# Performance work log

Measured on AMD Instinct MI355X. Metric: run time of the kernel, lower is better.

Reference implementation:

```python
import jax, jax.numpy as jnp
import numpy as np

VOCAB, B, T, E, H, C = 50000, 1024, 120, 50, 300, 5
FORGET_BIAS = 1.0  # tf.nn.rnn_cell.LSTMCell default


def setup_inputs() -> dict:
    key = jax.random.key(0)
    ks = jax.random.split(key, 8)
    tokens = jax.random.randint(ks[0], (B, T, 1), 0, VOCAB, dtype=jnp.int32)
    labels = jax.random.randint(ks[1], (B, T), 0, C, dtype=jnp.int32)
    mask = jax.random.randint(ks[2], (B, T), 0, 2, dtype=jnp.int32).astype(bool)
    embeddings = jax.random.normal(ks[3], (VOCAB, E), dtype=jnp.float32) * 0.1
    Wx = jax.random.normal(ks[4], (E, 4 * H), dtype=jnp.float32) * (1.0 / np.sqrt(E))
    Wh = jax.random.normal(ks[5], (H, 4 * H), dtype=jnp.float32) * (1.0 / np.sqrt(H))
    b = jnp.zeros((4 * H,), dtype=jnp.float32)
    U = jax.random.normal(ks[6], (H, C), dtype=jnp.float32) * (1.0 / np.sqrt(H))
    b2 = jnp.zeros((C,), dtype=jnp.float32)
    return {"tokens": tokens, "labels": labels, "mask": mask,
            "embeddings": embeddings, "Wx": Wx, "Wh": Wh, "b": b, "U": U, "b2": b2}


def reference(tokens, labels, mask, embeddings, Wx, Wh, b, U, b2):
    # Embedding lookup: (B, T, n_features=1) -> (B, T, E)
    x = embeddings[tokens[..., 0]]

    def step(carry, xt):
        c, h = carry
        z = xt @ Wx + h @ Wh + b           # (B, 4H), gate order i, j, f, o
        i, j, f, o = jnp.split(z, 4, axis=-1)
        c_new = jax.nn.sigmoid(f + FORGET_BIAS) * c + jax.nn.sigmoid(i) * jnp.tanh(j)
        h_new = jax.nn.sigmoid(o) * jnp.tanh(c_new)
        return (c_new, h_new), h_new

    nb = x.shape[0]
    c0 = jnp.zeros((nb, H), dtype=x.dtype)
    h0 = jnp.zeros((nb, H), dtype=x.dtype)
    _, hs = jax.lax.scan(step, (c0, h0), jnp.swapaxes(x, 0, 1))  # (T, B, H)
    hs = jnp.swapaxes(hs, 0, 1)                                   # (B, T, H)

    logits = hs @ U + b2                                          # (B, T, C)
    logp = jax.nn.log_softmax(logits, axis=-1)
    ce = -jnp.take_along_axis(logp, labels[..., None].astype(jnp.int32), axis=-1)[..., 0]
    m = mask.astype(ce.dtype)
    loss = jnp.sum(ce * m) / jnp.sum(m)  # mean over unmasked tokens
    return loss
```

## Files before the change

kernel.cpp:

```cpp
#include <hip/hip_runtime.h>
#include <hip/hip_bf16.h>
#include <math.h>

#define NBATCH 1024
#define NT 120
#define NE 50
#define NH 300
#define NC 5
#define GH 1200
#define NKPAD 352
#define NSTRIP 15
#define HS 20
#define SCOL 80
#define NGRP 16
#define BB 64
#define ASTR 360
#define WSTR 360
#define ZSTR 84
#define HBSTR 304
#define HCH 76
#define NCHUNK 4800

typedef __attribute__((ext_vector_type(8))) short short8;
typedef __attribute__((ext_vector_type(4))) float f32x4;
typedef __attribute__((ext_vector_type(2))) unsigned short us2;

static __device__ __forceinline__ float bf2f(unsigned short u) {
    unsigned int x = ((unsigned int)u) << 16;
    return __builtin_bit_cast(float, x);
}
static __device__ __forceinline__ unsigned short f2bf(float f) {
    __hip_bfloat16 h = __float2bfloat16(f);
    return __builtin_bit_cast(unsigned short, h);
}

__global__ __launch_bounds__(256)
void wswz_kernel(const float* __restrict__ Wx, const float* __restrict__ Wh,
                 unsigned short* __restrict__ Wswz)
{
    int idx = blockIdx.x * 256 + threadIdx.x;
    if (idx >= NSTRIP * SCOL * NKPAD) return;
    int s = idx / (SCOL * NKPAD);
    int r = idx % (SCOL * NKPAD);
    int j = r / NKPAD, k = r % NKPAD;
    int col = (j & 3) * NH + s * HS + (j >> 2);
    float v = 0.f;
    if (k < NH)           v = Wh[k * GH + col];
    else if (k < NH + NE) v = Wx[(k - NH) * GH + col];
    Wswz[idx] = f2bf(v);
}

__device__ __forceinline__ void load_h(const unsigned short* __restrict__ hb,
                                       int b0, unsigned short* A_s, int tid)
{
    const unsigned long long* src =
        (const unsigned long long*)(hb + (size_t)b0 * HBSTR);
    unsigned long long v[19];
#pragma unroll
    for (int m = 0; m < 19; ++m) {
        const int idx = tid + 256 * m;
        if (idx < NCHUNK) {
            const int row = idx / 75, j = idx % 75;
            v[m] = __hip_atomic_load(src + (size_t)row * HCH + j,
                                     __ATOMIC_RELAXED, __HIP_MEMORY_SCOPE_AGENT);
        }
    }
#pragma unroll
    for (int m = 0; m < 19; ++m) {
        const int idx = tid + 256 * m;
        if (idx < NCHUNK) {
            const int row = idx / 75, j = idx % 75;
            *(unsigned long long*)(A_s + row * ASTR + j * 4) = v[m];
        }
    }
}

__device__ __forceinline__ void store_h(unsigned short* hb, int b0, int st,
                                        const unsigned short* h_stage, int tid)
{
#pragma unroll
    for (int m = 0; m < 2; ++m) {
        const int c = tid + m * 256;
        if (c < 320) {
            const int row = c / 5, j = c % 5;
            unsigned long long val =
                *(const unsigned long long*)(h_stage + row * HS + j * 4);
            unsigned long long* p = (unsigned long long*)
                (hb + (size_t)(b0 + row) * HBSTR + st * HS + j * 4);
            __hip_atomic_store(p, val, __ATOMIC_RELAXED,
                               __HIP_MEMORY_SCOPE_AGENT);
        }
    }
}

__device__ __forceinline__ void load_x(const int* __restrict__ tokens,
                                       const float* __restrict__ emb,
                                       int b0, int t, unsigned short* A_s, int tid)
{
    const int row = tid >> 2, q = tid & 3;
    const int tok = tokens[(b0 + row) * NT + t];
    const float* er = emb + (size_t)tok * NE;
    unsigned short* dst = A_s + row * ASTR + NH;
    for (int m = 0; m < 7; ++m) {
        int f = q + 4 * m;
        if (f < 25) {
            float2 v = *(const float2*)(er + f * 2);
            us2 o; o.x = f2bf(v.x); o.y = f2bf(v.y);
            *(us2*)(dst + f * 2) = o;
        }
    }
}

__device__ __forceinline__ void do_ce(bool doCE, int tc, int b0, int r0, int nr,
        const unsigned short* A_s, const float* U_s, const float* __restrict__ b2,
        const int* __restrict__ labels, const int* __restrict__ mask,
        float* __restrict__ ce_arr, float* llds, float* lgl, int tid)
{
    if (doCE && tid < nr * 50) {
        int i = tid / 50, rem = tid % 50, c = rem / 10, q = rem % 10;
        const unsigned short* ar = A_s + (r0 + i) * ASTR + q * 30;
        const float* up = U_s + q * 30 * NC + c;
        float acc = 0.f;
#pragma unroll
        for (int k = 0; k < 30; ++k) acc += bf2f(ar[k]) * up[k * NC];
        llds[i * 50 + c * 10 + q] = acc;
    }
    __syncthreads();
    if (doCE && tid < nr * NC) {
        int i = tid / NC, c = tid % NC;
        const float* pp = llds + i * 50 + c * 10;
        float sum = pp[0]+pp[1]+pp[2]+pp[3]+pp[4]+pp[5]+pp[6]+pp[7]+pp[8]+pp[9];
        lgl[i * NC + c] = sum + b2[c];
    }
    __syncthreads();
    if (doCE && tid < nr) {
        const float* L = lgl + tid * NC;
        float m = fmaxf(fmaxf(fmaxf(L[0], L[1]), fmaxf(L[2], L[3])), L[4]);
        float ssum = expf(L[0]-m)+expf(L[1]-m)+expf(L[2]-m)+expf(L[3]-m)+expf(L[4]-m);
        float lse = m + logf(ssum);
        int bidx = b0 + r0 + tid;
        int lab = labels[bidx * NT + tc];
        int mk  = mask[bidx * NT + tc];
        ce_arr[bidx * NT + tc] = mk ? (lse - L[lab]) : 0.f;
    }
}

__global__ __launch_bounds__(256, 1)
void lstm_persist(const int* __restrict__ tokens,
                  const int* __restrict__ labels,
                  const int* __restrict__ mask,
                  const float* __restrict__ emb,
                  const float* __restrict__ bias,
                  const float* __restrict__ U,
                  const float* __restrict__ b2,
                  const unsigned short* __restrict__ Wswz,
                  unsigned short* __restrict__ hbuf,
                  float* __restrict__ ce_arr,
                  int* __restrict__ flags)
{
    __shared__ unsigned short A_s[BB * ASTR];
    __shared__ unsigned short W_s[SCOL * WSTR];
    __shared__ __align__(16) unsigned short h_stage[BB * HS];
    __shared__ float z_s[BB * ZSTR];
    __shared__ float c_s[BB * HS];
    __shared__ float U_s[NH * NC];
    __shared__ float b_s[SCOL];
    __shared__ float llds[5 * 50];
    __shared__ float lgl[32];

    const int tid  = threadIdx.x;
    const int g    = blockIdx.x & 15;
    const int s    = blockIdx.x >> 4;
    const int b0   = g * BB;
    const int wave = tid >> 6;
    const int lane = tid & 63;
    const int c15  = lane & 15;
    const int kq   = lane >> 4;
    const int r0   = (s * BB) / NSTRIP;
    const int r1   = ((s + 1) * BB) / NSTRIP;
    const int nr   = r1 - r0;

    for (int idx = tid; idx < SCOL * 44; idx += 256) {
        int j = idx / 44, ch = idx % 44;
        *(uint4*)(W_s + j * WSTR + ch * 8) =
            *(const uint4*)(Wswz + (size_t)s * SCOL * NKPAD + j * NKPAD + ch * 8);
    }
    for (int idx = tid; idx < BB * NH; idx += 256) {
        int row = idx / NH, k = idx % NH;
        A_s[row * ASTR + k] = 0;
    }
    for (int idx = tid; idx < BB * 10; idx += 256) {
        int row = idx / 10, k = 350 + idx % 10;
        A_s[row * ASTR + k] = 0;
    }
    for (int idx = tid; idx < BB * HS; idx += 256) c_s[idx] = 0.f;
    for (int idx = tid; idx < NH * NC; idx += 256) U_s[idx] = U[idx];
    if (tid < SCOL) b_s[tid] = bias[(tid & 3) * NH + s * HS + (tid >> 2)];
    load_x(tokens, emb, b0, 0, A_s, tid);
    __syncthreads();

    const unsigned short* Ab = A_s + (wave * 16 + c15) * ASTR + kq * 8;
    const unsigned short* Wb = W_s + c15 * WSTR + kq * 8;

    for (int t = 0; t < NT; ++t) {
        f32x4 acc[5];
#pragma unroll
        for (int n = 0; n < 5; ++n) acc[n] = (f32x4){0.f, 0.f, 0.f, 0.f};
#pragma unroll
        for (int ks = 0; ks < 11; ++ks) {
            short8 av = *(const short8*)(Ab + ks * 32);
#pragma unroll
            for (int n = 0; n < 5; ++n) {
                short8 bv = *(const short8*)(Wb + n * 16 * WSTR + ks * 32);
                acc[n] = __builtin_amdgcn_mfma_f32_16x16x32_bf16(av, bv, acc[n], 0, 0, 0);
            }
        }
#pragma unroll
        for (int n = 0; n < 5; ++n)
#pragma unroll
            for (int j = 0; j < 4; ++j)
                z_s[(wave * 16 + kq * 4 + j) * ZSTR + n * 16 + c15] = acc[n][j];
        __syncthreads();

#pragma unroll
        for (int ii = 0; ii < 5; ++ii) {
            int idx = tid * 5 + ii;
            int row = idx / HS, h = idx % HS;
            f32x4 z4 = *(f32x4*)(z_s + row * ZSTR + h * 4);
            float zi = z4[0] + b_s[4 * h + 0];
            float zj = z4[1] + b_s[4 * h + 1];
            float zf = z4[2] + b_s[4 * h + 2];
            float zo = z4[3] + b_s[4 * h + 3];
            float co = c_s[idx];
            float fg = 1.f / (1.f + expf(-(zf + 1.f)));
            float ig = 1.f / (1.f + expf(-zi));
            float og = 1.f / (1.f + expf(-zo));
            float cn = fg * co + ig * tanhf(zj);
            float hn = og * tanhf(cn);
            c_s[idx] = cn;
            h_stage[idx] = f2bf(hn);
        }
        __syncthreads();

        unsigned short* hb = hbuf + (size_t)(t & 1) * (NBATCH * HBSTR);
        store_h(hb, b0, s, h_stage, tid);
        asm volatile("s_waitcnt vmcnt(0)" ::: "memory");
        __syncthreads();

        if (tid == 0)
            __hip_atomic_store(flags + (size_t)(t * NGRP + g) * 16 + s, 1,
                               __ATOMIC_RELAXED, __HIP_MEMORY_SCOPE_AGENT);

        if (t + 1 < NT) load_x(tokens, emb, b0, t + 1, A_s, tid);
        do_ce(t >= 1, t - 1, b0, r0, nr, A_s, U_s, b2, labels, mask,
              ce_arr, llds, lgl, tid);

        if (tid < NSTRIP) {
            const int* fp = flags + (size_t)(t * NGRP + g) * 16 + tid;
            int fv = 0; int gu = 0;
            do {
                fv = __hip_atomic_load(fp, __ATOMIC_RELAXED,
                                       __HIP_MEMORY_SCOPE_AGENT);
                if (!fv) __builtin_amdgcn_s_sleep(4);
            } while (!fv && ++gu < (1 << 17));
        }
        __syncthreads();

        load_h(hb, b0, A_s, tid);
        __syncthreads();
    }

    do_ce(true, NT - 1, b0, r0, nr, A_s, U_s, b2, labels, mask,
          ce_arr, llds, lgl, tid);
}

__global__ __launch_bounds__(256)
void reduce1_kernel(const float* __restrict__ ce_arr,
                    const int* __restrict__ mask,
                    float* __restrict__ pce, float* __restrict__ pm)
{
    __shared__ float s_ce[256];
    __shared__ float s_m[256];
    const int tid = threadIdx.x;
    const int lo = blockIdx.x * 480;
    float ac = 0.f, am = 0.f;
    for (int i = lo + tid; i < lo + 480; i += 256) {
        ac += ce_arr[i];
        am += (float)mask[i];
    }
    s_ce[tid] = ac; s_m[tid] = am;
    __syncthreads();
    for (int r = 128; r > 0; r >>= 1) {
        if (tid < r) { s_ce[tid] += s_ce[tid + r]; s_m[tid] += s_m[tid + r]; }
        __syncthreads();
    }
    if (tid == 0) { pce[blockIdx.x] = s_ce[0]; pm[blockIdx.x] = s_m[0]; }
}

__global__ __launch_bounds__(256)
void reduce2_kernel(const float* __restrict__ pce,
                    const float* __restrict__ pm,
                    float* __restrict__ out)
{
    __shared__ float s_ce[256];
    __shared__ float s_m[256];
    const int tid = threadIdx.x;
    s_ce[tid] = pce[tid];
    s_m[tid]  = pm[tid];
    __syncthreads();
    for (int r = 128; r > 0; r >>= 1) {
        if (tid < r) { s_ce[tid] += s_ce[tid + r]; s_m[tid] += s_m[tid + r]; }
        __syncthreads();
    }
    if (tid == 0) out[0] = s_ce[0] / s_m[0];
}

extern "C" void kernel_launch(void* const* d_in, const int* in_sizes, int n_in,
                              void* d_out, int out_size, void* d_ws, size_t ws_size,
                              hipStream_t stream)
{
    const int*   tokens = (const int*)d_in[0];
    const int*   labels = (const int*)d_in[1];
    const int*   mask   = (const int*)d_in[2];
    const float* emb    = (const float*)d_in[3];
    const float* Wx     = (const float*)d_in[4];
    const float* Wh     = (const float*)d_in[5];
    const float* bias   = (const float*)d_in[6];
    const float* U      = (const float*)d_in[7];
    const float* b2     = (const float*)d_in[8];

    char* wsb = (char*)d_ws;
    unsigned short* Wswz = (unsigned short*)wsb;
    unsigned short* hbuf = (unsigned short*)(wsb + 844800);
    float* ce    = (float*)(wsb + 2089984);
    float* pce   = (float*)(wsb + 2581504);
    float* pm    = (float*)(wsb + 2582528);
    int*   flags = (int*)(wsb + 2583552);

    hipMemsetAsync(flags, 0, 122880, stream);
    wswz_kernel<<<(NSTRIP * SCOL * NKPAD + 255) / 256, 256, 0, stream>>>(Wx, Wh, Wswz);
    lstm_persist<<<NGRP * NSTRIP, 256, 0, stream>>>(
        tokens, labels, mask, emb, bias, U, b2, Wswz, hbuf, ce, flags);
    reduce1_kernel<<<256, 256, 0, stream>>>(ce, mask, pce, pm);
    reduce2_kernel<<<1, 256, 0, stream>>>(pce, pm, (float*)d_out);
}
```

Baseline: 787.6 us.

## Hold weights in registers and compute output logits with MFMA

The persistent LSTM kernel now loads its weight slice straight into registers (55 short8 fragments per lane) rather than staging it in LDS. This removes the per-step LDS reads of W inside the recurrent matmul. The scalar cross-entropy stage, which used LDS partial sums and two extra barriers, becomes a single MFMA against a pre-swizzled bf16 U, followed by shuffle-based log-softmax. The cost is much higher register pressure, which risks spills at one block per CU. Each block also now computes logits for all 64 rows and masks the writes to its own row range, and the logits use bf16 U instead of fp32.

```diff
diff --git a/kernel.cpp b/kernel.cpp
--- a/kernel.cpp
+++ b/kernel.cpp
@@ -15,7 +15,6 @@
 #define NGRP 16
 #define BB 64
 #define ASTR 360
-#define WSTR 360
 #define ZSTR 84
 #define HBSTR 304
 #define HCH 76
@@ -50,6 +49,16 @@
     Wswz[idx] = f2bf(v);
 }
 
+__global__ __launch_bounds__(256)
+void uswz_kernel(const float* __restrict__ U, unsigned short* __restrict__ Uswz)
+{
+    int idx = blockIdx.x * 256 + threadIdx.x;
+    if (idx >= 16 * NKPAD) return;
+    int c = idx / NKPAD, k = idx % NKPAD;
+    float v = (c < NC && k < NH) ? U[k * NC + c] : 0.f;
+    Uswz[idx] = f2bf(v);
+}
+
 __device__ __forceinline__ void load_h(const unsigned short* __restrict__ hb,
                                        int b0, unsigned short* A_s, int tid)
 {
@@ -111,62 +120,24 @@
     }
 }
 
-__device__ __forceinline__ void do_ce(bool doCE, int tc, int b0, int r0, int nr,
-        const unsigned short* A_s, const float* U_s, const float* __restrict__ b2,
-        const int* __restrict__ labels, const int* __restrict__ mask,
-        float* __restrict__ ce_arr, float* llds, float* lgl, int tid)
-{
-    if (doCE && tid < nr * 50) {
-        int i = tid / 50, rem = tid % 50, c = rem / 10, q = rem % 10;
-        const unsigned short* ar = A_s + (r0 + i) * ASTR + q * 30;
-        const float* up = U_s + q * 30 * NC + c;
-        float acc = 0.f;
-#pragma unroll
-        for (int k = 0; k < 30; ++k) acc += bf2f(ar[k]) * up[k * NC];
-        llds[i * 50 + c * 10 + q] = acc;
-    }
-    __syncthreads();
-    if (doCE && tid < nr * NC) {
-        int i = tid / NC, c = tid % NC;
-        const float* pp = llds + i * 50 + c * 10;
-        float sum = pp[0]+pp[1]+pp[2]+pp[3]+pp[4]+pp[5]+pp[6]+pp[7]+pp[8]+pp[9];
-        lgl[i * NC + c] = sum + b2[c];
-    }
-    __syncthreads();
-    if (doCE && tid < nr) {
-        const float* L = lgl + tid * NC;
-        float m = fmaxf(fmaxf(fmaxf(L[0], L[1]), fmaxf(L[2], L[3])), L[4]);
-        float ssum = expf(L[0]-m)+expf(L[1]-m)+expf(L[2]-m)+expf(L[3]-m)+expf(L[4]-m);
-        float lse = m + logf(ssum);
-        int bidx = b0 + r0 + tid;
-        int lab = labels[bidx * NT + tc];
-        int mk  = mask[bidx * NT + tc];
-        ce_arr[bidx * NT + tc] = mk ? (lse - L[lab]) : 0.f;
-    }
-}
-
 __global__ __launch_bounds__(256, 1)
 void lstm_persist(const int* __restrict__ tokens,
                   const int* __restrict__ labels,
                   const int* __restrict__ mask,
                   const float* __restrict__ emb,
                   const float* __restrict__ bias,
-                  const float* __restrict__ U,
                   const float* __restrict__ b2,
                   const unsigned short* __restrict__ Wswz,
+                  const unsigned short* __restrict__ Uswz,
                   unsigned short* __restrict__ hbuf,
                   float* __restrict__ ce_arr,
                   int* __restrict__ flags)
 {
     __shared__ unsigned short A_s[BB * ASTR];
-    __shared__ unsigned short W_s[SCOL * WSTR];
     __shared__ __align__(16) unsigned short h_stage[BB * HS];
     __shared__ float z_s[BB * ZSTR];
     __shared__ float c_s[BB * HS];
-    __shared__ float U_s[NH * NC];
     __shared__ float b_s[SCOL];
-    __shared__ float llds[5 * 50];
-    __shared__ float lgl[32];
 
     const int tid  = threadIdx.x;
     const int g    = blockIdx.x & 15;
@@ -178,13 +149,24 @@
     const int kq   = lane >> 4;
     const int r0   = (s * BB) / NSTRIP;
     const int r1   = ((s + 1) * BB) / NSTRIP;
-    const int nr   = r1 - r0;
-
-    for (int idx = tid; idx < SCOL * 44; idx += 256) {
-        int j = idx / 44, ch = idx % 44;
-        *(uint4*)(W_s + j * WSTR + ch * 8) =
-            *(const uint4*)(Wswz + (size_t)s * SCOL * NKPAD + j * NKPAD + ch * 8);
-    }
+
+    short8 wv[11][5];
+    short8 uv[11];
+    {
+        const unsigned short* wb =
+            Wswz + (size_t)s * SCOL * NKPAD + kq * 8;
+#pragma unroll
+        for (int ks = 0; ks < 11; ++ks)
+#pragma unroll
+            for (int n = 0; n < 5; ++n)
+                wv[ks][n] = *(const short8*)(wb + (n * 16 + c15) * NKPAD + ks * 32);
+        const unsigned short* ub = Uswz + c15 * NKPAD + kq * 8;
+#pragma unroll
+        for (int ks = 0; ks < 11; ++ks)
+            uv[ks] = *(const short8*)(ub + ks * 32);
+    }
+    const float b2r = (c15 < NC) ? b2[c15] : 0.f;
+
     for (int idx = tid; idx < BB * NH; idx += 256) {
         int row = idx / NH, k = idx % NH;
         A_s[row * ASTR + k] = 0;
@@ -194,13 +176,11 @@
         A_s[row * ASTR + k] = 0;
     }
     for (int idx = tid; idx < BB * HS; idx += 256) c_s[idx] = 0.f;
-    for (int idx = tid; idx < NH * NC; idx += 256) U_s[idx] = U[idx];
     if (tid < SCOL) b_s[tid] = bias[(tid & 3) * NH + s * HS + (tid >> 2)];
     load_x(tokens, emb, b0, 0, A_s, tid);
     __syncthreads();
 
     const unsigned short* Ab = A_s + (wave * 16 + c15) * ASTR + kq * 8;
-    const unsigned short* Wb = W_s + c15 * WSTR + kq * 8;
 
     for (int t = 0; t < NT; ++t) {
         f32x4 acc[5];
@@ -210,10 +190,8 @@
         for (int ks = 0; ks < 11; ++ks) {
             short8 av = *(const short8*)(Ab + ks * 32);
 #pragma unroll
-            for (int n = 0; n < 5; ++n) {
-                short8 bv = *(const short8*)(Wb + n * 16 * WSTR + ks * 32);
-                acc[n] = __builtin_amdgcn_mfma_f32_16x16x32_bf16(av, bv, acc[n], 0, 0, 0);
-            }
+            for (int n = 0; n < 5; ++n)
+                acc[n] = __builtin_amdgcn_mfma_f32_16x16x32_bf16(av, wv[ks][n], acc[n], 0, 0, 0);
         }
 #pragma unroll
         for (int n = 0; n < 5; ++n)
@@ -252,8 +230,39 @@
                                __ATOMIC_RELAXED, __HIP_MEMORY_SCOPE_AGENT);
 
         if (t + 1 < NT) load_x(tokens, emb, b0, t + 1, A_s, tid);
-        do_ce(t >= 1, t - 1, b0, r0, nr, A_s, U_s, b2, labels, mask,
-              ce_arr, llds, lgl, tid);
+        if (t >= 1) {
+            const int tc = t - 1;
+            f32x4 accL = (f32x4){0.f, 0.f, 0.f, 0.f};
+#pragma unroll
+            for (int ks = 0; ks < 11; ++ks) {
+                short8 av = *(const short8*)(Ab + ks * 32);
+                accL = __builtin_amdgcn_mfma_f32_16x16x32_bf16(av, uv[ks], accL, 0, 0, 0);
+            }
+#pragma unroll
+            for (int j = 0; j < 4; ++j) {
+                float Lv = accL[j] + b2r;
+                float vm = (c15 < NC) ? Lv : -3.0e38f;
+#pragma unroll
+                for (int d = 1; d < 16; d <<= 1)
+                    vm = fmaxf(vm, __shfl_xor(vm, d, 16));
+                float p = (c15 < NC) ? expf(Lv - vm) : 0.f;
+                float sm = p;
+#pragma unroll
+                for (int d = 1; d < 16; d <<= 1)
+                    sm += __shfl_xor(sm, d, 16);
+                float lse = vm + logf(sm);
+                int row = wave * 16 + kq * 4 + j;
+                int inr = (row >= r0) && (row < r1);
+                int bidx = b0 + row;
+                int lab = (c15 == 0 && inr) ? labels[bidx * NT + tc] : 0;
+                int labb = __shfl(lab, 0, 16);
+                float ll = __shfl(Lv, labb, 16);
+                if (c15 == 0 && inr) {
+                    int mk = mask[bidx * NT + tc];
+                    ce_arr[bidx * NT + tc] = mk ? (lse - ll) : 0.f;
+                }
+            }
+        }
 
         if (tid < NSTRIP) {
             const int* fp = flags + (size_t)(t * NGRP + g) * 16 + tid;
@@ -270,8 +279,39 @@
         __syncthreads();
     }
 
-    do_ce(true, NT - 1, b0, r0, nr, A_s, U_s, b2, labels, mask,
-          ce_arr, llds, lgl, tid);
+    {
+        const int tc = NT - 1;
+        f32x4 accL = (f32x4){0.f, 0.f, 0.f, 0.f};
+#pragma unroll
+        for (int ks = 0; ks < 11; ++ks) {
+            short8 av = *(const short8*)(Ab + ks * 32);
+            accL = __builtin_amdgcn_mfma_f32_16x16x32_bf16(av, uv[ks], accL, 0, 0, 0);
+        }
+#pragma unroll
+        for (int j = 0; j < 4; ++j) {
+            float Lv = accL[j] + b2r;
+            float vm = (c15 < NC) ? Lv : -3.0e38f;
+#pragma unroll
+            for (int d = 1; d < 16; d <<= 1)
+                vm = fmaxf(vm, __shfl_xor(vm, d, 16));
+            float p = (c15 < NC) ? expf(Lv - vm) : 0.f;
+            float sm = p;
+#pragma unroll
+            for (int d = 1; d < 16; d <<= 1)
+                sm += __shfl_xor(sm, d, 16);
+            float lse = vm + logf(sm);
+            int row = wave * 16 + kq * 4 + j;
+            int inr = (row >= r0) && (row < r1);
+            int bidx = b0 + row;
+            int lab = (c15 == 0 && inr) ? labels[bidx * NT + tc] : 0;
+            int labb = __shfl(lab, 0, 16);
+            float ll = __shfl(Lv, labb, 16);
+            if (c15 == 0 && inr) {
+                int mk = mask[bidx * NT + tc];
+                ce_arr[bidx * NT + tc] = mk ? (lse - ll) : 0.f;
+            }
+        }
+    }
 }
 
 __global__ __launch_bounds__(256)
@@ -336,11 +376,13 @@
     float* pce   = (float*)(wsb + 2581504);
     float* pm    = (float*)(wsb + 2582528);
     int*   flags = (int*)(wsb + 2583552);
+    unsigned short* Uswz = (unsigned short*)(wsb + 2706432);
 
     hipMemsetAsync(flags, 0, 122880, stream);
     wswz_kernel<<<(NSTRIP * SCOL * NKPAD + 255) / 256, 256, 0, stream>>>(Wx, Wh, Wswz);
+    uswz_kernel<<<(16 * NKPAD + 255) / 256, 256, 0, stream>>>(U, Uswz);
     lstm_persist<<<NGRP * NSTRIP, 256, 0, stream>>>(
-        tokens, labels, mask, emb, bias, U, b2, Wswz, hbuf, ce, flags);
+        tokens, labels, mask, emb, bias, b2, Wswz, Uswz, hbuf, ce, flags);
     reduce1_kernel<<<256, 256, 0, stream>>>(ce, mask, pce, pm);
     reduce2_kernel<<<1, 256, 0, stream>>>(pce, pm, (float*)d_out);
 }
```

Result: slower. 1.027 ms (+30.4%).
